# Performance work log

Measured on AMD Instinct MI355X. Metric: run time of the kernel, lower is better.

The kernel has to match this reference:

```python
import jax, jax.numpy as jnp
import numpy as np

N = 100000
E = 1600000
F_IN = 100
H = 64
C = 18
K = 2  # num_stacks
T = 2  # num_layers


def setup_inputs() -> dict:
    key = jax.random.key(0)
    ks = jax.random.split(key, 12)
    def glorot(k, shape):
        fan = shape[-2] + shape[-1]
        s = jnp.sqrt(6.0 / fan)
        return jax.random.uniform(k, shape, jnp.float32, -s, s)
    return {
        "x": jax.random.normal(ks[0], (N, F_IN), jnp.float32),
        "edge_index": jax.random.randint(ks[1], (2, E), 0, N, jnp.int64),
        "init_w1": glorot(ks[2], (K, F_IN, H)),
        "w1": glorot(ks[3], (K, H, H)),
        "root_w1": glorot(ks[4], (K, F_IN, H)),
        "b1": jnp.zeros((K, 1, H), jnp.float32),
        "init_w2": glorot(ks[5], (K, H, C)),
        "w2": glorot(ks[6], (K, C, C)),
        "root_w2": glorot(ks[7], (K, H, C)),
        "b2": jnp.zeros((K, 1, C), jnp.float32),
    }


def _gcn_norm(src, tgt):
    # symmetric normalization, no self loops (PyG ARMAConv default)
    deg = jax.ops.segment_sum(jnp.ones((E,), jnp.float32), tgt, num_segments=N)
    dis = jnp.where(deg > 0, jax.lax.rsqrt(jnp.maximum(deg, 1.0)), 0.0)
    return dis[src] * dis[tgt]  # [E]


def _arma_conv(x, src, tgt, norm, init_w, w, root_w, b):
    # x: [N, Fin]; returns [N, Fout]
    root = jnp.einsum('nf,kfh->knh', x, root_w)  # [K, N, Fout] (shared across layers)
    out = None
    for t in range(T):
        if t == 0:
            h = jnp.einsum('nf,kfh->knh', x, init_w)
        else:
            h = jnp.einsum('knh,khg->kng', out, w)
        # gather-scale-scatter propagation per stack
        msgs = h[:, src, :] * norm[None, :, None]  # [K, E, Fout]
        agg = jax.vmap(lambda m: jax.ops.segment_sum(m, tgt, num_segments=N))(msgs)
        out = jax.nn.relu(agg + root + b)
    return out.mean(axis=0)  # mean over stacks


def reference(x, edge_index, init_w1, w1, root_w1, b1, init_w2, w2, root_w2, b2):
    src, tgt = edge_index[0], edge_index[1]
    norm = _gcn_norm(src, tgt)
    h = jax.nn.relu(_arma_conv(x, src, tgt, norm, init_w1, w1, root_w1, b1))
    out = _arma_conv(h, src, tgt, norm, init_w2, w2, root_w2, b2)
    return jax.nn.log_softmax(out, axis=-1)
```

## Files before the change

kernel.cpp:

```cpp
#include <hip/hip_runtime.h>
#include <hip/hip_bf16.h>
#include <math.h>

#define N_NODES 100000
#define N_EDGES 1600000
#define F_IN 100
#define H 64
#define C 18
#define BSHIFT 8
#define BSIZE 256
#define NBUCKETS ((N_NODES + BSIZE - 1) >> BSHIFT)
#define NBLK 256
#define CHUNK (N_EDGES / NBLK)

typedef __attribute__((ext_vector_type(8))) short v8s;
typedef __attribute__((ext_vector_type(4))) float v4f;
typedef __attribute__((ext_vector_type(2))) float v2f;


__device__ __forceinline__ unsigned bf16_rne(float f) {
    unsigned u = __float_as_uint(f);
    return (u + 0x7FFFu + ((u >> 16) & 1u)) >> 16;
}
__device__ __forceinline__ unsigned pack_bf2(float a, float b) {
    return bf16_rne(a) | (bf16_rne(b) << 16);
}
__device__ __forceinline__ float2 unpack_bf2(unsigned u) {
    return make_float2(__uint_as_float(u << 16), __uint_as_float(u & 0xFFFF0000u));
}
__device__ __forceinline__ ushort pack_fp8x2(float a, float b) {
    int r = __builtin_amdgcn_cvt_pk_fp8_f32(a, b, 0, false);
    return (ushort)(r & 0xFFFF);
}
__device__ __forceinline__ float2 unpack_fp8x2(ushort u) {
    v2f r = __builtin_amdgcn_cvt_pk_f32_fp8((int)u, false);
    return make_float2(r[0], r[1]);
}


__global__ void scan1_kernel(const int* __restrict__ cnt, int* __restrict__ excl,
                             int* __restrict__ bsum, int n) {
    __shared__ int tmp[256];
    int t = threadIdx.x;
    int i = blockIdx.x * 256 + t;
    int v = (i < n) ? cnt[i] : 0;
    tmp[t] = v;
    __syncthreads();
    for (int off = 1; off < 256; off <<= 1) {
        int xv = (t >= off) ? tmp[t - off] : 0;
        __syncthreads();
        tmp[t] += xv;
        __syncthreads();
    }
    if (i < n) excl[i] = tmp[t] - v;
    if (t == 255) bsum[blockIdx.x] = tmp[255];
}

__global__ void __launch_bounds__(512) scan2p_prep_kernel(
        int* __restrict__ bsum, int nb,
        const float* __restrict__ iw1, const float* __restrict__ rw1,
        const float* __restrict__ w1,  const float* __restrict__ iw2,
        const float* __restrict__ rw2, const float* __restrict__ w2,
        ushort* __restrict__ W1T, ushort* __restrict__ WmT,
        ushort* __restrict__ W2T, ushort* __restrict__ W3T) {
    int t = threadIdx.x;
    if (blockIdx.x == 0) {
        __shared__ int s[512];
        int v = (t < nb) ? bsum[t] : 0;
        s[t] = v;
        __syncthreads();
        for (int off = 1; off < 512; off <<= 1) {
            int xv = (t >= off) ? s[t - off] : 0;
            __syncthreads();
            s[t] += xv;
            __syncthreads();
        }
        if (t < nb) bsum[t] = s[t] - v;
        return;
    }
    int gid = (blockIdx.x - 1) * 512 + t;
    if (gid < 32768) {
        int idx = gid;
        int m = idx >> 13, nn = (idx >> 7) & 63, kk = idx & 127;
        int stk = m & 1, isWr = m >> 1;
        float v = 0.f;
        if (kk < F_IN) v = (isWr ? rw1 : iw1)[((size_t)stk * F_IN + kk) * 64 + nn];
        W1T[idx] = (ushort)bf16_rne(v);
    } else if (gid < 32768 + 8192) {
        int idx = gid - 32768;
        int stk = idx >> 12, g = (idx >> 6) & 63, f = idx & 63;
        WmT[idx] = (ushort)bf16_rne(w1[((size_t)stk * 64 + f) * 64 + g]);
    } else if (gid < 32768 + 8192 + 8192) {
        int idx = gid - 32768 - 8192;
        int m = idx >> 11, col = (idx >> 6) & 31, k = idx & 63;
        int stk = m & 1, isWr = m >> 1;
        float v = 0.f;
        if (col < C) v = (isWr ? rw2 : iw2)[((size_t)stk * H + k) * C + col];
        W2T[idx] = (ushort)bf16_rne(v);
    } else if (gid < 32768 + 8192 + 8192 + 2048) {
        int idx = gid - 32768 - 8192 - 8192;
        int stk = idx >> 10, col = (idx >> 5) & 31, k = idx & 31;
        float v = 0.f;
        if (col < C && k < C) v = w2[((size_t)stk * C + k) * C + col];
        W3T[idx] = (ushort)bf16_rne(v);
    }
}

__global__ void scan3_kernel(int* __restrict__ arr, const int* __restrict__ bsum,
                             int n, int sent) {
    int i = blockIdx.x * 256 + threadIdx.x;
    if (i < n) arr[i] += bsum[i >> 8];
    if (i == n && sent >= 0) arr[n] = sent;
}


__global__ void __launch_bounds__(256) histA_kernel(const int* __restrict__ tgt,
                                                    int* __restrict__ hist) {
    __shared__ int h[NBUCKETS];
    int blk = blockIdx.x, t = threadIdx.x;
    for (int i = t; i < NBUCKETS; i += 256) h[i] = 0;
    __syncthreads();
    int e0 = blk * CHUNK, e1 = e0 + CHUNK;
    for (int e = e0 + t; e < e1; e += 256) atomicAdd(&h[tgt[e] >> BSHIFT], 1);
    __syncthreads();
    for (int i = t; i < NBUCKETS; i += 256) hist[i * NBLK + blk] = h[i];
}

__global__ void __launch_bounds__(256) scatterC_kernel(
        const int* __restrict__ src, const int* __restrict__ tgt,
        const int* __restrict__ histx, unsigned* __restrict__ tmp) {
    __shared__ int cur[NBUCKETS];
    int blk = blockIdx.x, t = threadIdx.x;
    for (int i = t; i < NBUCKETS; i += 256) cur[i] = histx[i * NBLK + blk];
    __syncthreads();
    int e0 = blk * CHUNK, e1 = e0 + CHUNK;
    for (int e = e0 + t; e < e1; e += 256) {
        int s = src[e], tg = tgt[e];
        int b = tg >> BSHIFT;
        int pos = atomicAdd(&cur[b], 1);
        tmp[pos] = (unsigned)s | ((unsigned)(tg & (BSIZE - 1)) << 17);
    }
}

__global__ void __launch_bounds__(256) bucketD2_kernel(
        const unsigned* __restrict__ tmp, const int* __restrict__ histx,
        int* __restrict__ rp, float* __restrict__ dinv, int* __restrict__ ssrc) {
    __shared__ int cnt_l[BSIZE];
    __shared__ int scan_l[BSIZE];
    int b = blockIdx.x;
    int t = threadIdx.x;
    int e_lo = histx[(size_t)b * NBLK];
    int e_hi = (b + 1 < NBUCKETS) ? histx[(size_t)(b + 1) * NBLK] : N_EDGES;
    int n_lo = b << BSHIFT;
    int n_hi = min(n_lo + BSIZE, N_NODES);
    int nn = n_hi - n_lo;
    cnt_l[t] = 0;
    __syncthreads();
    for (int e = e_lo + t; e < e_hi; e += 256)
        atomicAdd(&cnt_l[(int)(tmp[e] >> 17)], 1);
    __syncthreads();
    int v = cnt_l[t];
    scan_l[t] = v;
    __syncthreads();
    for (int off = 1; off < 256; off <<= 1) {
        int xv = (t >= off) ? scan_l[t - off] : 0;
        __syncthreads();
        scan_l[t] += xv;
        __syncthreads();
    }
    int my_start = e_lo + scan_l[t] - v;
    if (t < nn) {
        rp[n_lo + t] = my_start;
        dinv[n_lo + t] = (v > 0) ? rsqrtf((float)v) : 0.f;
    }
    if (b == NBUCKETS - 1 && t == 0) rp[N_NODES] = N_EDGES;
    __syncthreads();
    cnt_l[t] = my_start;
    __syncthreads();
    for (int e = e_lo + t; e < e_hi; e += 256) {
        unsigned p = tmp[e];
        int s = (int)(p & 0x1FFFFu);
        int tl = (int)(p >> 17);
        int pos = atomicAdd(&cnt_l[tl], 1);
        ssrc[pos] = s;
    }
}


__global__ void __launch_bounds__(256) dense1_mfma(
        const float* __restrict__ x, const ushort* __restrict__ W1T,
        const float* __restrict__ dinv,
        ushort* __restrict__ g, ushort* __restrict__ root) {
    __shared__ char xs[32 * 256];
    int tid = threadIdx.x;
    int b0 = blockIdx.x * 32;
    for (int i = tid; i < 32 * 25; i += 256) {
        int row = i / 25, f4 = i - row * 25;
        int grow = b0 + row;
        float4 v = make_float4(0.f, 0.f, 0.f, 0.f);
        if (grow < N_NODES) v = *(const float4*)(x + (size_t)grow * F_IN + f4 * 4);
        unsigned p0 = pack_bf2(v.x, v.y);
        unsigned p1 = pack_bf2(v.z, v.w);
        int pr = f4 * 2;
        int gr = (pr >> 2) ^ (row & 7);
        char* base = xs + row * 256 + (gr << 4) + (pr & 3) * 4;
        *(unsigned*)base = p0;
        *(unsigned*)(base + 4) = p1;
    }
    for (int i = tid; i < 32 * 14; i += 256) {
        int row = i / 14, pr = 50 + (i - row * 14);
        int gr = (pr >> 2) ^ (row & 7);
        *(unsigned*)(xs + row * 256 + (gr << 4) + (pr & 3) * 4) = 0;
    }
    __syncthreads();
    int lane = tid & 63;
    int w = __builtin_amdgcn_readfirstlane(tid >> 6);
    int q = lane >> 4, cl = lane & 15;
    int isWr = w >> 1;
    int colbase = (w & 1) * 32;
    v8s bfr[2][2][4];
    #pragma unroll
    for (int stk = 0; stk < 2; ++stk)
        #pragma unroll
        for (int nt = 0; nt < 2; ++nt)
            #pragma unroll
            for (int ks = 0; ks < 4; ++ks) {
                const ushort* p = W1T + ((size_t)(isWr * 2 + stk) * 64 + colbase + nt * 16 + cl) * 128
                                  + ks * 32 + q * 8;
                bfr[stk][nt][ks] = *(const v8s*)p;
            }
    #pragma unroll
    for (int mt = 0; mt < 2; ++mt) {
        v8s afr[4];
        #pragma unroll
        for (int ks = 0; ks < 4; ++ks) {
            int row = mt * 16 + cl;
            int gr = (ks * 4 + q) ^ (row & 7);
            afr[ks] = *(const v8s*)(xs + row * 256 + (gr << 4));
        }
        v4f acc[2][2];
        #pragma unroll
        for (int stk = 0; stk < 2; ++stk)
            #pragma unroll
            for (int nt = 0; nt < 2; ++nt) {
                v4f a = {0.f, 0.f, 0.f, 0.f};
                #pragma unroll
                for (int ks = 0; ks < 4; ++ks)
                    a = __builtin_amdgcn_mfma_f32_16x16x32_bf16(afr[ks], bfr[stk][nt][ks], a, 0, 0, 0);
                acc[stk][nt] = a;
            }
        #pragma unroll
        for (int nt = 0; nt < 2; ++nt)
            #pragma unroll
            for (int reg = 0; reg < 4; ++reg) {
                int node = b0 + mt * 16 + q * 4 + reg;
                if (node < N_NODES) {
                    int col = colbase + nt * 16 + cl;
                    if (isWr == 0) {
                        float dv = dinv[node];
                        g[(size_t)node * 64 + col] = pack_fp8x2(dv * acc[0][nt][reg], dv * acc[1][nt][reg]);
                    } else {
                        root[(size_t)node * 64 + col] = pack_fp8x2(acc[0][nt][reg], acc[1][nt][reg]);
                    }
                }
            }
    }
}

__global__ void __launch_bounds__(256) dense_mid_mfma(
        const ushort* __restrict__ hk0, const ushort* __restrict__ hk1,
        const ushort* __restrict__ WmT, const float* __restrict__ dinv,
        ushort* __restrict__ g2) {
    __shared__ char hs[2 * 64 * 128];
    int tid = threadIdx.x;
    int b0 = blockIdx.x * 64;
    for (int i = tid; i < 1024; i += 256) {
        int stk = i >> 9, rem = i & 511, row = rem >> 3, gr = rem & 7;
        int grow = b0 + row;
        uint4 v = make_uint4(0, 0, 0, 0);
        const ushort* srcp = stk ? hk1 : hk0;
        if (grow < N_NODES) v = *(const uint4*)(srcp + (size_t)grow * 64 + gr * 8);
        *(uint4*)(hs + stk * 8192 + row * 128 + ((gr ^ (row & 7)) << 4)) = v;
    }
    __syncthreads();
    int lane = tid & 63;
    int w = __builtin_amdgcn_readfirstlane(tid >> 6);
    int q = lane >> 4, cl = lane & 15;
    v8s bfr[2][2];
    #pragma unroll
    for (int stk = 0; stk < 2; ++stk)
        #pragma unroll
        for (int ks = 0; ks < 2; ++ks)
            bfr[stk][ks] = *(const v8s*)(WmT + ((size_t)stk * 64 + w * 16 + cl) * 64 + ks * 32 + q * 8);
    #pragma unroll
    for (int mt = 0; mt < 4; ++mt) {
        v4f acc[2];
        #pragma unroll
        for (int stk = 0; stk < 2; ++stk) {
            v4f a = {0.f, 0.f, 0.f, 0.f};
            #pragma unroll
            for (int ks = 0; ks < 2; ++ks) {
                int row = mt * 16 + cl;
                int gr = (ks * 4 + q) ^ (row & 7);
                v8s af = *(const v8s*)(hs + stk * 8192 + row * 128 + (gr << 4));
                a = __builtin_amdgcn_mfma_f32_16x16x32_bf16(af, bfr[stk][ks], a, 0, 0, 0);
            }
            acc[stk] = a;
        }
        #pragma unroll
        for (int reg = 0; reg < 4; ++reg) {
            int node = b0 + mt * 16 + q * 4 + reg;
            if (node < N_NODES) {
                float dv = dinv[node];
                g2[(size_t)node * 64 + w * 16 + cl] = pack_fp8x2(dv * acc[0][reg], dv * acc[1][reg]);
            }
        }
    }
}

__global__ void __launch_bounds__(256) dense_y2_mfma(
        const ushort* __restrict__ yb, const ushort* __restrict__ W2T,
        const float* __restrict__ dinv,
        ushort* __restrict__ h2, unsigned* __restrict__ root2) {
    __shared__ char ys[64 * 128];
    int tid = threadIdx.x;
    int b0 = blockIdx.x * 64;
    for (int i = tid; i < 512; i += 256) {
        int row = i >> 3, gr = i & 7;
        int grow = b0 + row;
        uint4 v = make_uint4(0, 0, 0, 0);
        if (grow < N_NODES) v = *(const uint4*)(yb + (size_t)grow * 64 + gr * 8);
        *(uint4*)(ys + row * 128 + ((gr ^ (row & 7)) << 4)) = v;
    }
    __syncthreads();
    int lane = tid & 63;
    int w = __builtin_amdgcn_readfirstlane(tid >> 6);
    int q = lane >> 4, cl = lane & 15;
    int isWr = w >> 1;
    int mbase = (w & 1) * 2;
    v8s bfr[2][2][2];
    #pragma unroll
    for (int stk = 0; stk < 2; ++stk)
        #pragma unroll
        for (int nt = 0; nt < 2; ++nt)
            #pragma unroll
            for (int ks = 0; ks < 2; ++ks)
                bfr[stk][nt][ks] = *(const v8s*)(W2T + ((size_t)(isWr * 2 + stk) * 32 + nt * 16 + cl) * 64
                                                 + ks * 32 + q * 8);
    #pragma unroll
    for (int mi = 0; mi < 2; ++mi) {
        int mt = mbase + mi;
        v8s afr[2];
        #pragma unroll
        for (int ks = 0; ks < 2; ++ks) {
            int row = mt * 16 + cl;
            int gr = (ks * 4 + q) ^ (row & 7);
            afr[ks] = *(const v8s*)(ys + row * 128 + (gr << 4));
        }
        v4f acc[2][2];
        #pragma unroll
        for (int stk = 0; stk < 2; ++stk)
            #pragma unroll
            for (int nt = 0; nt < 2; ++nt) {
                v4f a = {0.f, 0.f, 0.f, 0.f};
                #pragma unroll
                for (int ks = 0; ks < 2; ++ks)
                    a = __builtin_amdgcn_mfma_f32_16x16x32_bf16(afr[ks], bfr[stk][nt][ks], a, 0, 0, 0);
                acc[stk][nt] = a;
            }
        #pragma unroll
        for (int nt = 0; nt < 2; ++nt)
            #pragma unroll
            for (int reg = 0; reg < 4; ++reg) {
                int node = b0 + mt * 16 + q * 4 + reg;
                int col = nt * 16 + cl;
                if (node < N_NODES && col < C) {
                    if (isWr == 0) {
                        float dv = dinv[node];
                        h2[(size_t)node * C + col] = pack_fp8x2(dv * acc[0][nt][reg], dv * acc[1][nt][reg]);
                    } else {
                        root2[(size_t)node * C + col] = pack_bf2(acc[0][nt][reg], acc[1][nt][reg]);
                    }
                }
            }
    }
}

__global__ void __launch_bounds__(256) dense_last_mfma(
        const ushort* __restrict__ ok0, const ushort* __restrict__ ok1,
        const ushort* __restrict__ W3T, const float* __restrict__ dinv,
        ushort* __restrict__ h3) {
    __shared__ char hs[2 * 64 * 64];
    int tid = threadIdx.x;
    int b0 = blockIdx.x * 64;
    for (int i = tid; i < 2048; i += 256) ((unsigned*)hs)[i] = 0;
    __syncthreads();
    for (int i = tid; i < 4096; i += 256) {
        int stk = i >> 11, row = (i >> 5) & 63, col = i & 31;
        int node = b0 + row;
        if (col < C && node < N_NODES) {
            ushort v = (stk ? ok1 : ok0)[(size_t)node * C + col];
            int gr = (col >> 3) ^ (row & 3);
            *(ushort*)(hs + stk * 4096 + row * 64 + (gr << 4) + (col & 7) * 2) = v;
        }
    }
    __syncthreads();
    int lane = tid & 63;
    int w = __builtin_amdgcn_readfirstlane(tid >> 6);
    int q = lane >> 4, cl = lane & 15;
    v8s bfr[2][2];
    #pragma unroll
    for (int stk = 0; stk < 2; ++stk)
        #pragma unroll
        for (int nt = 0; nt < 2; ++nt)
            bfr[stk][nt] = *(const v8s*)(W3T + ((size_t)stk * 32 + nt * 16 + cl) * 32 + q * 8);
    int row = w * 16 + cl;
    int gr = q ^ (row & 3);
    v8s af0 = *(const v8s*)(hs + row * 64 + (gr << 4));
    v8s af1 = *(const v8s*)(hs + 4096 + row * 64 + (gr << 4));
    v4f acc[2][2];
    #pragma unroll
    for (int nt = 0; nt < 2; ++nt) {
        acc[0][nt] = __builtin_amdgcn_mfma_f32_16x16x32_bf16(af0, bfr[0][nt], (v4f){0.f,0.f,0.f,0.f}, 0, 0, 0);
        acc[1][nt] = __builtin_amdgcn_mfma_f32_16x16x32_bf16(af1, bfr[1][nt], (v4f){0.f,0.f,0.f,0.f}, 0, 0, 0);
    }
    #pragma unroll
    for (int nt = 0; nt < 2; ++nt)
        #pragma unroll
        for (int reg = 0; reg < 4; ++reg) {
            int node = b0 + w * 16 + q * 4 + reg;
            int col = nt * 16 + cl;
            if (node < N_NODES && col < C) {
                float dv = dinv[node];
                h3[(size_t)node * C + col] = pack_fp8x2(dv * acc[0][nt][reg], dv * acc[1][nt][reg]);
            }
        }
}


template <int FINAL>
__global__ void __launch_bounds__(256) prop64_kernel(
        const ushort* __restrict__ g, const ushort* __restrict__ root,
        const float* __restrict__ b, const float* __restrict__ dinv,
        const int* __restrict__ rp, const int* __restrict__ ssrc,
        ushort* __restrict__ ok0, ushort* __restrict__ ok1, ushort* __restrict__ yb) {
    int lane = threadIdx.x & 63;
    int wid = __builtin_amdgcn_readfirstlane((int)((blockIdx.x * 256 + threadIdx.x) >> 6));
    if (wid >= N_NODES) return;
    int e0 = rp[wid], e1 = rp[wid + 1];
    ushort rtu = root[(size_t)wid * H + lane];
    float dv = dinv[wid];
    float bl0 = b[lane], bl1 = b[H + lane];
    float a0 = 0.f, a1 = 0.f;
    int e = e0;
    for (; e + 8 <= e1; e += 8) {
        ushort u[8];
        #pragma unroll
        for (int j = 0; j < 8; ++j) u[j] = g[(size_t)ssrc[e + j] * H + lane];
        #pragma unroll
        for (int j = 0; j < 8; ++j) { float2 v = unpack_fp8x2(u[j]); a0 += v.x; a1 += v.y; }
    }
    for (; e < e1; ++e) {
        float2 v = unpack_fp8x2(g[(size_t)ssrc[e] * H + lane]);
        a0 += v.x; a1 += v.y;
    }
    float2 rt = unpack_fp8x2(rtu);
    float o0 = fmaxf(fmaf(dv, a0, rt.x + bl0), 0.f);
    float o1 = fmaxf(fmaf(dv, a1, rt.y + bl1), 0.f);
    if (FINAL) {
        yb[(size_t)wid * H + lane] = (ushort)bf16_rne(0.5f * (o0 + o1));
    } else {
        ok0[(size_t)wid * H + lane] = (ushort)bf16_rne(o0);
        ok1[(size_t)wid * H + lane] = (ushort)bf16_rne(o1);
    }
}

template <int FINAL>
__global__ void __launch_bounds__(256) prop18_kernel(
        const ushort* __restrict__ g, const unsigned* __restrict__ root,
        const float* __restrict__ b, const float* __restrict__ dinv,
        const int* __restrict__ rp, const int* __restrict__ ssrc,
        ushort* __restrict__ ok0, ushort* __restrict__ ok1, float* __restrict__ outp) {
    int lane = threadIdx.x & 63;
    int wid = __builtin_amdgcn_readfirstlane((int)((blockIdx.x * 256 + threadIdx.x) >> 6));
    if (wid >= N_NODES) return;
    int e0 = rp[wid], e1 = rp[wid + 1];
    bool hi = lane >= 32;
    int c32 = lane & 31;
    bool actG = c32 < C;
    int c = actG ? c32 : 0;
    unsigned rtu = root[(size_t)wid * C + c];
    float dv = dinv[wid];
    float bl0 = b[c], bl1 = b[C + c];
    float a0 = 0.f, a1 = 0.f;
    int e = e0;
    for (; e + 16 <= e1; e += 16) {
        ushort u[8];
        #pragma unroll
        for (int j = 0; j < 8; ++j) {
            int s0 = ssrc[e + 2 * j];
            int s1 = ssrc[e + 2 * j + 1];
            int srow = hi ? s1 : s0;
            u[j] = g[(size_t)srow * C + c];
        }
        if (actG) {
            #pragma unroll
            for (int j = 0; j < 8; ++j) { float2 v = unpack_fp8x2(u[j]); a0 += v.x; a1 += v.y; }
        }
    }
    for (; e + 2 <= e1; e += 2) {
        int s0 = ssrc[e];
        int s1 = ssrc[e + 1];
        int srow = hi ? s1 : s0;
        float2 v = unpack_fp8x2(g[(size_t)srow * C + c]);
        if (actG) { a0 += v.x; a1 += v.y; }
    }
    if (e < e1) {
        int s0 = ssrc[e];
        float2 v = unpack_fp8x2(g[(size_t)s0 * C + c]);
        if (actG && !hi) { a0 += v.x; a1 += v.y; }
    }
    a0 += __shfl_xor(a0, 32, 64);
    a1 += __shfl_xor(a1, 32, 64);
    bool actO = lane < C;
    if (!FINAL) {
        if (actO) {
            float2 rt = unpack_bf2(rtu);
            float o0 = fmaxf(fmaf(dv, a0, rt.x + bl0), 0.f);
            float o1 = fmaxf(fmaf(dv, a1, rt.y + bl1), 0.f);
            ok0[(size_t)wid * C + c] = (ushort)bf16_rne(o0);
            ok1[(size_t)wid * C + c] = (ushort)bf16_rne(o1);
        }
    } else {
        float m = -INFINITY;
        if (actO) {
            float2 rt = unpack_bf2(rtu);
            float o0 = fmaxf(fmaf(dv, a0, rt.x + bl0), 0.f);
            float o1 = fmaxf(fmaf(dv, a1, rt.y + bl1), 0.f);
            m = 0.5f * (o0 + o1);
        }
        float mx = m;
        #pragma unroll
        for (int off = 16; off >= 1; off >>= 1) mx = fmaxf(mx, __shfl_xor(mx, off, 64));
        float ex = actO ? __expf(m - mx) : 0.f;
        float sum = ex;
        #pragma unroll
        for (int off = 16; off >= 1; off >>= 1) sum += __shfl_xor(sum, off, 64);
        if (actO) outp[(size_t)wid * C + c] = m - mx - logf(sum);
    }
}


extern "C" void kernel_launch(void* const* d_in, const int* in_sizes, int n_in,
                              void* d_out, int out_size, void* d_ws, size_t ws_size,
                              hipStream_t stream) {
    const float* x        = (const float*)d_in[0];
    const int*   ei       = (const int*)d_in[1];
    const float* init_w1  = (const float*)d_in[2];
    const float* w1       = (const float*)d_in[3];
    const float* root_w1  = (const float*)d_in[4];
    const float* b1       = (const float*)d_in[5];
    const float* init_w2  = (const float*)d_in[6];
    const float* w2       = (const float*)d_in[7];
    const float* root_w2  = (const float*)d_in[8];
    const float* b2       = (const float*)d_in[9];
    const int* src = ei;
    const int* tgt = ei + N_EDGES;
    float* out = (float*)d_out;

    char* w = (char*)d_ws;
    size_t off = 0;
    auto alloc = [&](size_t bytes) -> char* {
        char* p = w + off;
        off += (bytes + 255) & ~(size_t)255;
        return p;
    };
    int*      rp    = (int*)alloc((size_t)(N_NODES + 1) * 4);
    float*    dinv  = (float*)alloc((size_t)N_NODES * 4);
    int*      bsum  = (int*)alloc(512 * 4);
    int*      hist  = (int*)alloc((size_t)NBUCKETS * NBLK * 4);
    int*      histx = (int*)alloc((size_t)NBUCKETS * NBLK * 4);
    unsigned* tmp   = (unsigned*)alloc((size_t)N_EDGES * 4);
    int*      ssrc  = (int*)alloc((size_t)N_EDGES * 4);
    ushort*   W1T   = (ushort*)alloc((size_t)4 * 64 * 128 * 2);
    ushort*   WmT   = (ushort*)alloc((size_t)2 * 64 * 64 * 2);
    ushort*   W2T   = (ushort*)alloc((size_t)4 * 32 * 64 * 2);
    ushort*   W3T   = (ushort*)alloc((size_t)2 * 32 * 32 * 2);
    ushort*   g1    = (ushort*)alloc((size_t)N_NODES * H * 2);
    ushort*   root1 = (ushort*)alloc((size_t)N_NODES * H * 2);
    ushort*   hk0   = (ushort*)alloc((size_t)N_NODES * H * 2);
    ushort*   hk1   = (ushort*)alloc((size_t)N_NODES * H * 2);
    ushort*   g2    = (ushort*)alloc((size_t)N_NODES * H * 2);
    ushort*   yb    = (ushort*)alloc((size_t)N_NODES * H * 2);
    ushort*   h2u   = (ushort*)alloc((size_t)N_NODES * C * 2);
    unsigned* root2u= (unsigned*)alloc((size_t)N_NODES * C * 4);
    ushort*   h3u   = (ushort*)alloc((size_t)N_NODES * C * 2);
    ushort*   p18k0 = (ushort*)g1;
    ushort*   p18k1 = (ushort*)g1 + (size_t)N_NODES * C;

    int nbH = (NBUCKETS * NBLK + 255) / 256;

    histA_kernel<<<NBLK, 256, 0, stream>>>(tgt, hist);
    scan1_kernel<<<nbH, 256, 0, stream>>>(hist, histx, bsum, NBUCKETS * NBLK);
    scan2p_prep_kernel<<<101, 512, 0, stream>>>(bsum, nbH,
                                                init_w1, root_w1, w1, init_w2, root_w2, w2,
                                                W1T, WmT, W2T, W3T);
    scan3_kernel<<<nbH, 256, 0, stream>>>(histx, bsum, NBUCKETS * NBLK, -1);
    scatterC_kernel<<<NBLK, 256, 0, stream>>>(src, tgt, histx, tmp);
    bucketD2_kernel<<<NBUCKETS, 256, 0, stream>>>(tmp, histx, rp, dinv, ssrc);

    int g1blocks = (N_NODES + 31) / 32;
    int gblocks  = (N_NODES + 63) / 64;
    int pgrid    = (N_NODES + 3) / 4;

    dense1_mfma<<<g1blocks, 256, 0, stream>>>(x, W1T, dinv, g1, root1);
    prop64_kernel<0><<<pgrid, 256, 0, stream>>>(g1, root1, b1, dinv, rp, ssrc, hk0, hk1, nullptr);
    dense_mid_mfma<<<gblocks, 256, 0, stream>>>(hk0, hk1, WmT, dinv, g2);
    prop64_kernel<1><<<pgrid, 256, 0, stream>>>(g2, root1, b1, dinv, rp, ssrc, nullptr, nullptr, yb);

    dense_y2_mfma<<<gblocks, 256, 0, stream>>>(yb, W2T, dinv, h2u, root2u);
    prop18_kernel<0><<<pgrid, 256, 0, stream>>>(h2u, root2u, b2, dinv, rp, ssrc, p18k0, p18k1, nullptr);
    dense_last_mfma<<<gblocks, 256, 0, stream>>>(p18k0, p18k1, W3T, dinv, h3u);
    prop18_kernel<1><<<pgrid, 256, 0, stream>>>(h3u, root2u, b2, dinv, rp, ssrc, nullptr, nullptr, out);
}
```

Measured before the change: 311.7 us.

## Fold scan3 into consumers, widen prop64 gathers to two edges per wave, bf16 root

Drops the separate scan3 pass: scatterC and bucketD2 now add the block sums to histx on the fly, which saves one launch and a pass over the histogram. prop64 now has each wave handle two edges per iteration, with lanes 0-31 and 32-63 each loading a 32-bit word (two packed fp8x2 values) from a different source row. The two halves are combined with a cross-half shuffle, so the kernel issues fewer, wider gathers. The layer-1 root term is stored as bf16 pairs instead of fp8, which doubles its memory footprint and reads but improves precision.

```diff
diff --git a/kernel.cpp b/kernel.cpp
--- a/kernel.cpp
+++ b/kernel.cpp
@@ -106,13 +106,6 @@
     }
 }
 
-__global__ void scan3_kernel(int* __restrict__ arr, const int* __restrict__ bsum,
-                             int n, int sent) {
-    int i = blockIdx.x * 256 + threadIdx.x;
-    if (i < n) arr[i] += bsum[i >> 8];
-    if (i == n && sent >= 0) arr[n] = sent;
-}
-
 
 __global__ void __launch_bounds__(256) histA_kernel(const int* __restrict__ tgt,
                                                     int* __restrict__ hist) {
@@ -128,10 +121,14 @@
 
 __global__ void __launch_bounds__(256) scatterC_kernel(
         const int* __restrict__ src, const int* __restrict__ tgt,
-        const int* __restrict__ histx, unsigned* __restrict__ tmp) {
+        const int* __restrict__ histx, const int* __restrict__ bsum,
+        unsigned* __restrict__ tmp) {
     __shared__ int cur[NBUCKETS];
     int blk = blockIdx.x, t = threadIdx.x;
-    for (int i = t; i < NBUCKETS; i += 256) cur[i] = histx[i * NBLK + blk];
+    for (int i = t; i < NBUCKETS; i += 256) {
+        int gi = i * NBLK + blk;
+        cur[i] = histx[gi] + bsum[gi >> 8];
+    }
     __syncthreads();
     int e0 = blk * CHUNK, e1 = e0 + CHUNK;
     for (int e = e0 + t; e < e1; e += 256) {
@@ -144,13 +141,19 @@
 
 __global__ void __launch_bounds__(256) bucketD2_kernel(
         const unsigned* __restrict__ tmp, const int* __restrict__ histx,
+        const int* __restrict__ bsum,
         int* __restrict__ rp, float* __restrict__ dinv, int* __restrict__ ssrc) {
     __shared__ int cnt_l[BSIZE];
     __shared__ int scan_l[BSIZE];
     int b = blockIdx.x;
     int t = threadIdx.x;
-    int e_lo = histx[(size_t)b * NBLK];
-    int e_hi = (b + 1 < NBUCKETS) ? histx[(size_t)(b + 1) * NBLK] : N_EDGES;
+    int gi_lo = b * NBLK;
+    int e_lo = histx[gi_lo] + bsum[gi_lo >> 8];
+    int e_hi = N_EDGES;
+    if (b + 1 < NBUCKETS) {
+        int gi_hi = (b + 1) * NBLK;
+        e_hi = histx[gi_hi] + bsum[gi_hi >> 8];
+    }
     int n_lo = b << BSHIFT;
     int n_hi = min(n_lo + BSIZE, N_NODES);
     int nn = n_hi - n_lo;
@@ -190,7 +193,7 @@
 __global__ void __launch_bounds__(256) dense1_mfma(
         const float* __restrict__ x, const ushort* __restrict__ W1T,
         const float* __restrict__ dinv,
-        ushort* __restrict__ g, ushort* __restrict__ root) {
+        ushort* __restrict__ g, unsigned* __restrict__ root) {
     __shared__ char xs[32 * 256];
     int tid = threadIdx.x;
     int b0 = blockIdx.x * 32;
@@ -260,7 +263,7 @@
                         float dv = dinv[node];
                         g[(size_t)node * 64 + col] = pack_fp8x2(dv * acc[0][nt][reg], dv * acc[1][nt][reg]);
                     } else {
-                        root[(size_t)node * 64 + col] = pack_fp8x2(acc[0][nt][reg], acc[1][nt][reg]);
+                        root[(size_t)node * 64 + col] = pack_bf2(acc[0][nt][reg], acc[1][nt][reg]);
                     }
                 }
             }
@@ -440,7 +443,7 @@
 
 template <int FINAL>
 __global__ void __launch_bounds__(256) prop64_kernel(
-        const ushort* __restrict__ g, const ushort* __restrict__ root,
+        const ushort* __restrict__ g, const unsigned* __restrict__ root,
         const float* __restrict__ b, const float* __restrict__ dinv,
         const int* __restrict__ rp, const int* __restrict__ ssrc,
         ushort* __restrict__ ok0, ushort* __restrict__ ok1, ushort* __restrict__ yb) {
@@ -448,30 +451,67 @@
     int wid = __builtin_amdgcn_readfirstlane((int)((blockIdx.x * 256 + threadIdx.x) >> 6));
     if (wid >= N_NODES) return;
     int e0 = rp[wid], e1 = rp[wid + 1];
-    ushort rtu = root[(size_t)wid * H + lane];
+    bool hi = lane >= 32;
+    int c32 = lane & 31;
+    const unsigned* g32 = (const unsigned*)g;
+    uint2 rtu = *(const uint2*)(root + (size_t)wid * H + 2 * c32);
     float dv = dinv[wid];
-    float bl0 = b[lane], bl1 = b[H + lane];
-    float a0 = 0.f, a1 = 0.f;
+    float bA0 = b[2 * c32], bB0 = b[2 * c32 + 1];
+    float bA1 = b[H + 2 * c32], bB1 = b[H + 2 * c32 + 1];
+    float aA0 = 0.f, aA1 = 0.f, aB0 = 0.f, aB1 = 0.f;
     int e = e0;
-    for (; e + 8 <= e1; e += 8) {
-        ushort u[8];
-        #pragma unroll
-        for (int j = 0; j < 8; ++j) u[j] = g[(size_t)ssrc[e + j] * H + lane];
-        #pragma unroll
-        for (int j = 0; j < 8; ++j) { float2 v = unpack_fp8x2(u[j]); a0 += v.x; a1 += v.y; }
-    }
-    for (; e < e1; ++e) {
-        float2 v = unpack_fp8x2(g[(size_t)ssrc[e] * H + lane]);
-        a0 += v.x; a1 += v.y;
-    }
-    float2 rt = unpack_fp8x2(rtu);
-    float o0 = fmaxf(fmaf(dv, a0, rt.x + bl0), 0.f);
-    float o1 = fmaxf(fmaf(dv, a1, rt.y + bl1), 0.f);
-    if (FINAL) {
-        yb[(size_t)wid * H + lane] = (ushort)bf16_rne(0.5f * (o0 + o1));
-    } else {
-        ok0[(size_t)wid * H + lane] = (ushort)bf16_rne(o0);
-        ok1[(size_t)wid * H + lane] = (ushort)bf16_rne(o1);
+    for (; e + 16 <= e1; e += 16) {
+        unsigned u[8];
+        #pragma unroll
+        for (int j = 0; j < 8; ++j) {
+            int s0 = ssrc[e + 2 * j];
+            int s1 = ssrc[e + 2 * j + 1];
+            int srow = hi ? s1 : s0;
+            u[j] = g32[(size_t)srow * 32 + c32];
+        }
+        #pragma unroll
+        for (int j = 0; j < 8; ++j) {
+            float2 vA = unpack_fp8x2((ushort)(u[j] & 0xFFFFu));
+            float2 vB = unpack_fp8x2((ushort)(u[j] >> 16));
+            aA0 += vA.x; aA1 += vA.y; aB0 += vB.x; aB1 += vB.y;
+        }
+    }
+    for (; e + 2 <= e1; e += 2) {
+        int s0 = ssrc[e];
+        int s1 = ssrc[e + 1];
+        int srow = hi ? s1 : s0;
+        unsigned u = g32[(size_t)srow * 32 + c32];
+        float2 vA = unpack_fp8x2((ushort)(u & 0xFFFFu));
+        float2 vB = unpack_fp8x2((ushort)(u >> 16));
+        aA0 += vA.x; aA1 += vA.y; aB0 += vB.x; aB1 += vB.y;
+    }
+    if (e < e1) {
+        int s0 = ssrc[e];
+        unsigned u = g32[(size_t)s0 * 32 + c32];
+        if (!hi) {
+            float2 vA = unpack_fp8x2((ushort)(u & 0xFFFFu));
+            float2 vB = unpack_fp8x2((ushort)(u >> 16));
+            aA0 += vA.x; aA1 += vA.y; aB0 += vB.x; aB1 += vB.y;
+        }
+    }
+    aA0 += __shfl_xor(aA0, 32, 64);
+    aA1 += __shfl_xor(aA1, 32, 64);
+    aB0 += __shfl_xor(aB0, 32, 64);
+    aB1 += __shfl_xor(aB1, 32, 64);
+    if (lane < 32) {
+        float2 rtA = unpack_bf2(rtu.x);
+        float2 rtB = unpack_bf2(rtu.y);
+        float oA0 = fmaxf(fmaf(dv, aA0, rtA.x + bA0), 0.f);
+        float oA1 = fmaxf(fmaf(dv, aA1, rtA.y + bA1), 0.f);
+        float oB0 = fmaxf(fmaf(dv, aB0, rtB.x + bB0), 0.f);
+        float oB1 = fmaxf(fmaf(dv, aB1, rtB.y + bB1), 0.f);
+        size_t base = (size_t)wid * H + 2 * c32;
+        if (FINAL) {
+            *(unsigned*)(yb + base) = pack_bf2(0.5f * (oA0 + oA1), 0.5f * (oB0 + oB1));
+        } else {
+            *(unsigned*)(ok0 + base) = pack_bf2(oA0, oB0);
+            *(unsigned*)(ok1 + base) = pack_bf2(oA1, oB1);
+        }
     }
 }
 
@@ -587,7 +627,7 @@
     ushort*   W2T   = (ushort*)alloc((size_t)4 * 32 * 64 * 2);
     ushort*   W3T   = (ushort*)alloc((size_t)2 * 32 * 32 * 2);
     ushort*   g1    = (ushort*)alloc((size_t)N_NODES * H * 2);
-    ushort*   root1 = (ushort*)alloc((size_t)N_NODES * H * 2);
+    unsigned* root1 = (unsigned*)alloc((size_t)N_NODES * H * 4);
     ushort*   hk0   = (ushort*)alloc((size_t)N_NODES * H * 2);
     ushort*   hk1   = (ushort*)alloc((size_t)N_NODES * H * 2);
     ushort*   g2    = (ushort*)alloc((size_t)N_NODES * H * 2);
@@ -605,9 +645,8 @@
     scan2p_prep_kernel<<<101, 512, 0, stream>>>(bsum, nbH,
                                                 init_w1, root_w1, w1, init_w2, root_w2, w2,
                                                 W1T, WmT, W2T, W3T);
-    scan3_kernel<<<nbH, 256, 0, stream>>>(histx, bsum, NBUCKETS * NBLK, -1);
-    scatterC_kernel<<<NBLK, 256, 0, stream>>>(src, tgt, histx, tmp);
-    bucketD2_kernel<<<NBUCKETS, 256, 0, stream>>>(tmp, histx, rp, dinv, ssrc);
+    scatterC_kernel<<<NBLK, 256, 0, stream>>>(src, tgt, histx, bsum, tmp);
+    bucketD2_kernel<<<NBUCKETS, 256, 0, stream>>>(tmp, histx, bsum, rp, dinv, ssrc);
 
     int g1blocks = (N_NODES + 31) / 32;
     int gblocks  = (N_NODES + 63) / 64;
```

Measured after the change: 309.6 us (median of 2 runs). About the same (-0.7%).
